# Optimization experiments

Hardware: AMD Instinct MI355X
Metric: run time of the kernel (lower is better)

The kernel has to match this reference:

```python
import jax, jax.numpy as jnp
import numpy as np
from jax import lax

A = 20            # len(ANCHOR_RATIOS)=4 * len(ANCHOR_SCALES)=5 in neural-motifs config
TGT = 6           # anchor_target_dim
DIM = 512
IN_DIM = 1024
B, H, W = 16, 37, 37


def setup_inputs() -> dict:
    key = jax.random.key(0)
    k1, k2, k3, k4, k5 = jax.random.split(key, 5)
    fmap = jax.random.normal(k1, (B, IN_DIM, H, W), dtype=jnp.float32)
    # conv weights in OIHW, fan-in scaled init
    W1 = jax.random.normal(k2, (DIM, IN_DIM, 3, 3), dtype=jnp.float32) / np.sqrt(IN_DIM * 9)
    b1 = jnp.zeros((DIM,), dtype=jnp.float32)
    W2 = jax.random.normal(k3, (TGT * A, DIM, 1, 1), dtype=jnp.float32) / np.sqrt(DIM)
    b2 = jnp.zeros((TGT * A,), dtype=jnp.float32)
    return {"fmap": fmap, "W1": W1, "b1": b1, "W2": W2, "b2": b2}


def reference(fmap, W1, b1, W2, b2):
    dn = ("NCHW", "OIHW", "NCHW")
    # 3x3 conv, padding=1
    x = lax.conv_general_dilated(fmap, W1, window_strides=(1, 1), padding="SAME",
                                 dimension_numbers=dn) + b1[None, :, None, None]
    # ReLU6
    x = jnp.clip(x, 0.0, 6.0)
    # 1x1 conv -> [B, 6*A, H, W]
    x = lax.conv_general_dilated(x, W2, window_strides=(1, 1), padding="VALID",
                                 dimension_numbers=dn) + b2[None, :, None, None]
    # _reshape_channels: [B, C, H, W] -> [B, H, W, C], then split C -> (A, 6)
    b, c, h, w = x.shape
    x = jnp.transpose(x, (0, 2, 3, 1))
    return x.reshape(b, h, w, A, TGT)
```

## Files before the change

kernel.cpp:

```cpp
#include <hip/hip_runtime.h>
#include <stdint.h>

#define HW   1369
#define QW   39
#define QP   1616
#define QT   1536
#define CIN  1024
#define CMID 512
#define KTOT 9216
#define NTIL 144
#define ASL  12288
#define BB   24576
#define BSL  8192

typedef float  f32x4  __attribute__((ext_vector_type(4)));
typedef __bf16 bf16x8 __attribute__((ext_vector_type(8)));

__device__ __forceinline__ uint16_t f2bf(float f) {
  uint32_t u = __float_as_uint(f);
  u += 0x7fffu + ((u >> 16) & 1u);
  return (uint16_t)(u >> 16);
}

__device__ __forceinline__ void gll16(const void* g, void* l) {
  const __attribute__((address_space(1))) uint32_t* ga =
      (const __attribute__((address_space(1))) uint32_t*)(uintptr_t)g;
  __attribute__((address_space(3))) uint32_t* la =
      (__attribute__((address_space(3))) uint32_t*)(uint32_t)(uintptr_t)l;
  __builtin_amdgcn_global_load_lds(ga, la, 16, 0, 0);
}

__global__ void k_zero_border(uint16_t* __restrict__ Xp) {
  const int bx = blockIdx.x;
  const int batch = bx / 210, idx = bx - batch * 210;
  int q;
  if (idx < 40)       q = idx;
  else if (idx < 136) q = 1520 + (idx - 40);
  else {
    const int k = idx - 136;
    const int pair = k >> 1;
    q = (k & 1) ? ((pair + 1) * 39 + 38)
                : ((pair + 2) * 39);
  }
  uint64_t* p = (uint64_t*)(Xp + ((size_t)batch * QP + q) * CIN);
  p[threadIdx.x] = 0ull;
}

__global__ void k_pad_transpose(const float* __restrict__ fmap, uint16_t* __restrict__ Xp) {
  __shared__ float t[32][33];
  const int b = blockIdx.z;
  const int c0 = blockIdx.y * 32;
  const int p0 = blockIdx.x * 32;
  const int tx = threadIdx.x, ty = threadIdx.y;
  const float* src = fmap + ((size_t)b * CIN + c0) * HW + p0;
#pragma unroll
  for (int i = 0; i < 4; ++i) {
    int cc = ty + i * 8;
    t[cc][tx] = (p0 + tx < HW) ? src[(size_t)cc * HW + tx] : 0.f;
  }
  __syncthreads();
#pragma unroll
  for (int i = 0; i < 4; ++i) {
    int pl = ty + i * 8;
    int p = p0 + pl;
    if (p < HW) {
      int h = p / 37, w = p - h * 37;
      int q = (h + 1) * QW + (w + 1);
      Xp[((size_t)b * QP + q) * CIN + c0 + tx] = f2bf(t[tx][pl]);
    }
  }
}

__global__ void k_pack_w1(const float* __restrict__ W1, uint16_t* __restrict__ Apk) {
  int idx = blockIdx.x * 256 + threadIdx.x;
  if (idx >= 512 * KTOT) return;
  int o = idx / KTOT, k = idx - o * KTOT;
  int r = k >> 10, c = k & 1023;
  Apk[idx] = f2bf(W1[((size_t)o * CIN + c) * 9 + r]);
}

__global__ void k_pack_w2(const float* __restrict__ W2, uint16_t* __restrict__ W2p) {
  int idx = blockIdx.x * 256 + threadIdx.x;
  int j = idx >> 9, o = idx & 511;
  W2p[idx] = (j < 120) ? f2bf(W2[j * 512 + o]) : (uint16_t)0;
}

__global__ __launch_bounds__(256, 2) void k_conv1(
    const uint16_t* __restrict__ Xp, const uint16_t* __restrict__ Apk,
    const float* __restrict__ b1, uint16_t* __restrict__ x1) {
  __shared__ __align__(16) uint16_t lds[2 * ASL + 2 * BSL];

  const int tid  = threadIdx.x;
  const int wid  = tid >> 6, lane = tid & 63;
  const int lrow = lane & 15, lq = lane >> 4;
  const int wm   = wid >> 1,  wn = wid & 1;

  const int bid = blockIdx.x;
  const int g   = (bid & 7) * 64 + (bid >> 3);
  const int mt  = g >> 2, nt = g & 3;
  const int batch = mt >> 3, qb = (mt & 7) * 192;
  const int o0 = nt * 128;
  const uint16_t* Xb = Xp + (size_t)batch * QP * CIN;

  const int xorb    = (lrow & 7) << 4;
  const int col_el0 = ((lq * 16) ^ xorb) >> 1;
  const int col_el1 = col_el0 ^ 32;

  const int scol = ((tid & 7) ^ ((tid >> 3) & 7)) * 8;
  const int srow = tid >> 3;

  f32x4 acc[6][4] = {};

#define STAGE(u) do {                                                                 \
    if ((u) < NTIL) {                                                                 \
      const int cb_  = (u) / 9;                                                       \
      const int tap_ = (u) - cb_ * 9;                                                 \
      const int off_ = (tap_ / 3) * QW + tap_ % 3;                                    \
      const int c0_  = cb_ << 6;                                                      \
      uint16_t* sa = lds + ((u) & 1) * ASL;                                           \
      uint16_t* sb = lds + BB + ((u) & 1) * BSL;                                      \
      _Pragma("unroll")                                                               \
      for (int j = 0; j < 6; ++j)                                                     \
        gll16(Xb + (size_t)(qb + off_ + j * 32 + srow) * CIN + c0_ + scol,            \
              sa + (j * 256 + wid * 64) * 8);                                         \
      _Pragma("unroll")                                                               \
      for (int j = 0; j < 4; ++j)                                                     \
        gll16(Apk + (size_t)(o0 + j * 32 + srow) * KTOT + (tap_ << 10) + c0_ + scol,  \
              sb + (j * 256 + wid * 64) * 8);                                         \
    }                                                                                 \
  } while (0)

  STAGE(0);

  for (int t = 0; t < NTIL; ++t) {
    const uint16_t* As = lds + (t & 1) * ASL;
    const uint16_t* Bs = lds + BB + (t & 1) * BSL;
    asm volatile("s_waitcnt vmcnt(0)" ::: "memory");
    asm volatile("s_barrier" ::: "memory");
    __builtin_amdgcn_sched_barrier(0);
    STAGE(t + 1);

    bf16x8 av0[6], av1[6], bv0[4], bv1[4];
#pragma unroll
    for (int n = 0; n < 4; ++n) {
      const uint16_t* br = Bs + (wn * 64 + n * 16 + lrow) * 64;
      bv0[n] = *(const bf16x8*)(br + col_el0);
      bv1[n] = *(const bf16x8*)(br + col_el1);
    }
#pragma unroll
    for (int m = 0; m < 6; ++m) {
      const uint16_t* ar = As + (wm * 96 + m * 16 + lrow) * 64;
      av0[m] = *(const bf16x8*)(ar + col_el0);
      av1[m] = *(const bf16x8*)(ar + col_el1);
    }
    __builtin_amdgcn_s_setprio(1);
#pragma unroll
    for (int m = 0; m < 6; ++m)
#pragma unroll
      for (int n = 0; n < 4; ++n)
        acc[m][n] = __builtin_amdgcn_mfma_f32_16x16x32_bf16(av0[m], bv0[n], acc[m][n], 0, 0, 0);
#pragma unroll
    for (int m = 0; m < 6; ++m)
#pragma unroll
      for (int n = 0; n < 4; ++n)
        acc[m][n] = __builtin_amdgcn_mfma_f32_16x16x32_bf16(av1[m], bv1[n], acc[m][n], 0, 0, 0);
    __builtin_amdgcn_s_setprio(0);
  }

  const int qr = lq * 4;
#pragma unroll
  for (int n = 0; n < 4; ++n) {
    const int o = o0 + wn * 64 + n * 16 + lrow;
    const float bias = b1[o];
#pragma unroll
    for (int m = 0; m < 6; ++m) {
#pragma unroll
      for (int v = 0; v < 4; ++v) {
        const int q = qb + wm * 96 + m * 16 + qr + v;
        float x = acc[m][n][v] + bias;
        x = fminf(fmaxf(x, 0.f), 6.f);
        x1[((size_t)batch * QT + q) * CMID + o] = f2bf(x);
      }
    }
  }
#undef STAGE
}

__global__ __launch_bounds__(256, 2) void k_conv2(
    const uint16_t* __restrict__ x1, const uint16_t* __restrict__ W2p,
    const float* __restrict__ b2, float* __restrict__ out) {
  __shared__ __align__(16) uint16_t lA[64 * 64];
  __shared__ __align__(16) uint16_t lB[128 * 64];
  const int tid = threadIdx.x;
  const int wid = tid >> 6, lane = tid & 63;
  const int b = blockIdx.z, q0 = blockIdx.x * 64;
  const uint16_t* Ab = x1 + (size_t)b * QT * CMID;
  const int wm = wid >> 1, wn = wid & 1;
  const int lrow = lane & 15, lk = (lane >> 4) * 8;
  f32x4 acc[2][4] = {};

  for (int kt = 0; kt < 8; ++kt) {
    const int c0 = kt << 6;
#pragma unroll
    for (int i = 0; i < 2; ++i) {
      int wb = i * 256 + wid * 64;
      int chunk = wb + lane;
      int row = chunk >> 3, ch = chunk & 7;
      gll16(Ab + (size_t)(q0 + row) * CMID + c0 + ch * 8, lA + wb * 8);
    }
#pragma unroll
    for (int i = 0; i < 4; ++i) {
      int wb = i * 256 + wid * 64;
      int chunk = wb + lane;
      int row = chunk >> 3, ch = chunk & 7;
      gll16(W2p + (size_t)row * CMID + c0 + ch * 8, lB + wb * 8);
    }
    __syncthreads();
#pragma unroll
    for (int kk = 0; kk < 2; ++kk) {
      bf16x8 av[2], bv[4];
#pragma unroll
      for (int mi = 0; mi < 2; ++mi)
        av[mi] = *(const bf16x8*)(lA + (wm * 32 + mi * 16 + lrow) * 64 + kk * 32 + lk);
#pragma unroll
      for (int ni = 0; ni < 4; ++ni)
        bv[ni] = *(const bf16x8*)(lB + (wn * 64 + ni * 16 + lrow) * 64 + kk * 32 + lk);
#pragma unroll
      for (int mi = 0; mi < 2; ++mi)
#pragma unroll
        for (int ni = 0; ni < 4; ++ni)
          acc[mi][ni] = __builtin_amdgcn_mfma_f32_16x16x32_bf16(av[mi], bv[ni], acc[mi][ni], 0, 0, 0);
    }
    __syncthreads();
  }

  const int qr = (lane >> 4) * 4;
#pragma unroll
  for (int ni = 0; ni < 4; ++ni) {
    int j = wn * 64 + ni * 16 + lrow;
    if (j < 120) {
      float bias = b2[j];
#pragma unroll
      for (int mi = 0; mi < 2; ++mi) {
#pragma unroll
        for (int v = 0; v < 4; ++v) {
          int q = q0 + wm * 32 + mi * 16 + qr + v;
          int h = q / QW, w = q - h * QW;
          if (h < 37 && w < 37) {
            out[((size_t)b * HW + h * 37 + w) * 120 + j] = acc[mi][ni][v] + bias;
          }
        }
      }
    }
  }
}

extern "C" void kernel_launch(void* const* d_in, const int* in_sizes, int n_in,
                              void* d_out, int out_size, void* d_ws, size_t ws_size,
                              hipStream_t stream) {
  const float* fmap = (const float*)d_in[0];
  const float* W1   = (const float*)d_in[1];
  const float* b1   = (const float*)d_in[2];
  const float* W2   = (const float*)d_in[3];
  const float* b2   = (const float*)d_in[4];
  float* out = (float*)d_out;

  uint8_t* ws = (uint8_t*)d_ws;
  const size_t XP_BYTES  = (size_t)16 * QP * CIN * 2;
  const size_t W1P_BYTES = (size_t)512 * KTOT * 2;
  const size_t W2P_BYTES = (size_t)128 * 512 * 2;
  uint16_t* Xp  = (uint16_t*)ws;
  uint16_t* Apk = (uint16_t*)(ws + XP_BYTES);
  uint16_t* W2p = (uint16_t*)(ws + XP_BYTES + W1P_BYTES);
  uint16_t* x1  = (uint16_t*)(ws + XP_BYTES + W1P_BYTES + W2P_BYTES);

  k_zero_border<<<dim3(16 * 210), dim3(256), 0, stream>>>(Xp);
  k_pad_transpose<<<dim3(43, 32, 16), dim3(32, 8), 0, stream>>>(fmap, Xp);
  k_pack_w1<<<dim3((512 * KTOT + 255) / 256), dim3(256), 0, stream>>>(W1, Apk);
  k_pack_w2<<<dim3(256), dim3(256), 0, stream>>>(W2, W2p);
  k_conv1<<<dim3(512), dim3(256), 0, stream>>>(Xp, Apk, b1, x1);
  k_conv2<<<dim3(24, 1, 16), dim3(256), 0, stream>>>(x1, W2p, b2, out);
}
```

Baseline: 242.9 us.

## Reuse a per-channel-block input panel across all nine conv taps

```diff
diff --git a/kernel.cpp b/kernel.cpp
--- a/kernel.cpp
+++ b/kernel.cpp
@@ -3,14 +3,13 @@
 
 #define HW   1369
 #define QW   39
-#define QP   1616
+#define QP2  1648
 #define QT   1536
 #define CIN  1024
 #define CMID 512
 #define KTOT 9216
 #define NTIL 144
-#define ASL  12288
-#define BB   24576
+#define PANEL 18432
 #define BSL  8192
 
 typedef float  f32x4  __attribute__((ext_vector_type(4)));
@@ -39,10 +38,9 @@
   else {
     const int k = idx - 136;
     const int pair = k >> 1;
-    q = (k & 1) ? ((pair + 1) * 39 + 38)
-                : ((pair + 2) * 39);
-  }
-  uint64_t* p = (uint64_t*)(Xp + ((size_t)batch * QP + q) * CIN);
+    q = (k & 1) ? ((pair + 1) * 39 + 38) : ((pair + 2) * 39);
+  }
+  uint64_t* p = (uint64_t*)(Xp + ((size_t)batch * QP2 + q) * CIN);
   p[threadIdx.x] = 0ull;
 }
 
@@ -66,7 +64,7 @@
     if (p < HW) {
       int h = p / 37, w = p - h * 37;
       int q = (h + 1) * QW + (w + 1);
-      Xp[((size_t)b * QP + q) * CIN + c0 + tx] = f2bf(t[tx][pl]);
+      Xp[((size_t)b * QP2 + q) * CIN + c0 + tx] = f2bf(t[tx][pl]);
     }
   }
 }
@@ -88,7 +86,7 @@
 __global__ __launch_bounds__(256, 2) void k_conv1(
     const uint16_t* __restrict__ Xp, const uint16_t* __restrict__ Apk,
     const float* __restrict__ b1, uint16_t* __restrict__ x1) {
-  __shared__ __align__(16) uint16_t lds[2 * ASL + 2 * BSL];
+  __shared__ __align__(16) uint16_t lds[PANEL + 2 * BSL];
 
   const int tid  = threadIdx.x;
   const int wid  = tid >> 6, lane = tid & 63;
@@ -100,7 +98,7 @@
   const int mt  = g >> 2, nt = g & 3;
   const int batch = mt >> 3, qb = (mt & 7) * 192;
   const int o0 = nt * 128;
-  const uint16_t* Xb = Xp + (size_t)batch * QP * CIN;
+  const uint16_t* Xb = Xp + (size_t)batch * QP2 * CIN;
 
   const int xorb    = (lrow & 7) << 4;
   const int col_el0 = ((lq * 16) ^ xorb) >> 1;
@@ -109,62 +107,83 @@
   const int scol = ((tid & 7) ^ ((tid >> 3) & 7)) * 8;
   const int srow = tid >> 3;
 
+  const int sR8 = lane >> 3;
+  const int sc8 = ((lane & 7) ^ sR8) * 8;
+
   f32x4 acc[6][4] = {};
 
-#define STAGE(u) do {                                                                 \
-    if ((u) < NTIL) {                                                                 \
-      const int cb_  = (u) / 9;                                                       \
-      const int tap_ = (u) - cb_ * 9;                                                 \
-      const int off_ = (tap_ / 3) * QW + tap_ % 3;                                    \
-      const int c0_  = cb_ << 6;                                                      \
-      uint16_t* sa = lds + ((u) & 1) * ASL;                                           \
-      uint16_t* sb = lds + BB + ((u) & 1) * BSL;                                      \
-      _Pragma("unroll")                                                               \
-      for (int j = 0; j < 6; ++j)                                                     \
-        gll16(Xb + (size_t)(qb + off_ + j * 32 + srow) * CIN + c0_ + scol,            \
-              sa + (j * 256 + wid * 64) * 8);                                         \
-      _Pragma("unroll")                                                               \
-      for (int j = 0; j < 4; ++j)                                                     \
-        gll16(Apk + (size_t)(o0 + j * 32 + srow) * KTOT + (tap_ << 10) + c0_ + scol,  \
-              sb + (j * 256 + wid * 64) * 8);                                         \
+#define STPAN(cb1, call) do {                                                         \
+    if ((cb1) < 16) {                                                                 \
+      const int c0_ = (cb1) << 6;                                                     \
+      const int Rb  = (call) * 32 + wid * 8;                                          \
+      gll16(Xb + (size_t)(qb + Rb + sR8) * CIN + c0_ + sc8, lds + Rb * 64);           \
     }                                                                                 \
   } while (0)
 
-  STAGE(0);
-
-  for (int t = 0; t < NTIL; ++t) {
-    const uint16_t* As = lds + (t & 1) * ASL;
-    const uint16_t* Bs = lds + BB + (t & 1) * BSL;
-    asm volatile("s_waitcnt vmcnt(0)" ::: "memory");
-    asm volatile("s_barrier" ::: "memory");
-    __builtin_amdgcn_sched_barrier(0);
-    STAGE(t + 1);
-
-    bf16x8 av0[6], av1[6], bv0[4], bv1[4];
-#pragma unroll
-    for (int n = 0; n < 4; ++n) {
-      const uint16_t* br = Bs + (wn * 64 + n * 16 + lrow) * 64;
-      bv0[n] = *(const bf16x8*)(br + col_el0);
-      bv1[n] = *(const bf16x8*)(br + col_el1);
-    }
-#pragma unroll
-    for (int m = 0; m < 6; ++m) {
-      const uint16_t* ar = As + (wm * 96 + m * 16 + lrow) * 64;
-      av0[m] = *(const bf16x8*)(ar + col_el0);
-      av1[m] = *(const bf16x8*)(ar + col_el1);
-    }
-    __builtin_amdgcn_s_setprio(1);
-#pragma unroll
-    for (int m = 0; m < 6; ++m)
-#pragma unroll
-      for (int n = 0; n < 4; ++n)
-        acc[m][n] = __builtin_amdgcn_mfma_f32_16x16x32_bf16(av0[m], bv0[n], acc[m][n], 0, 0, 0);
-#pragma unroll
-    for (int m = 0; m < 6; ++m)
-#pragma unroll
-      for (int n = 0; n < 4; ++n)
-        acc[m][n] = __builtin_amdgcn_mfma_f32_16x16x32_bf16(av1[m], bv1[n], acc[m][n], 0, 0, 0);
-    __builtin_amdgcn_s_setprio(0);
+#define STAGEB(cbv, tapv, slot) do {                                                  \
+    const int c0_ = (cbv) << 6;                                                       \
+    uint16_t* sb = lds + PANEL + (slot) * BSL;                                        \
+    _Pragma("unroll")                                                                 \
+    for (int j = 0; j < 4; ++j)                                                       \
+      gll16(Apk + (size_t)(o0 + j * 32 + srow) * KTOT + ((tapv) << 10) + c0_ + scol,  \
+            sb + (j * 256 + wid * 64) * 8);                                           \
+  } while (0)
+
+#pragma unroll
+  for (int c = 0; c < 9; ++c) STPAN(0, c);
+  STAGEB(0, 0, 0);
+
+  for (int cb = 0; cb < 16; ++cb) {
+#pragma unroll
+    for (int tap = 0; tap < 9; ++tap) {
+      const int t = cb * 9 + tap;
+      asm volatile("s_waitcnt vmcnt(0)" ::: "memory");
+      asm volatile("s_barrier" ::: "memory");
+      __builtin_amdgcn_sched_barrier(0);
+      if (tap < 8)           STAGEB(cb, tap + 1, (t + 1) & 1);
+      else if (cb + 1 < 16)  STAGEB(cb + 1, 0, (t + 1) & 1);
+
+      const int off_ = (tap / 3) * QW + tap % 3;
+      const int r7   = (off_ + lrow) & 7;
+      const int ce0  = ((lq * 16) ^ (r7 << 4)) >> 1;
+      const int ce1  = ce0 ^ 32;
+      const uint16_t* Bs = lds + PANEL + (t & 1) * BSL;
+
+      bf16x8 av0[6], av1[6], bv0[4], bv1[4];
+#pragma unroll
+      for (int n = 0; n < 4; ++n) {
+        const uint16_t* br = Bs + (wn * 64 + n * 16 + lrow) * 64;
+        bv0[n] = *(const bf16x8*)(br + col_el0);
+        bv1[n] = *(const bf16x8*)(br + col_el1);
+      }
+#pragma unroll
+      for (int m = 0; m < 6; ++m) {
+        const uint16_t* ar = lds + (off_ + wm * 96 + m * 16 + lrow) * 64;
+        av0[m] = *(const bf16x8*)(ar + ce0);
+        av1[m] = *(const bf16x8*)(ar + ce1);
+      }
+      __builtin_amdgcn_s_setprio(1);
+#pragma unroll
+      for (int m = 0; m < 6; ++m)
+#pragma unroll
+        for (int n = 0; n < 4; ++n)
+          acc[m][n] = __builtin_amdgcn_mfma_f32_16x16x32_bf16(av0[m], bv0[n], acc[m][n], 0, 0, 0);
+#pragma unroll
+      for (int m = 0; m < 6; ++m)
+#pragma unroll
+        for (int n = 0; n < 4; ++n)
+          acc[m][n] = __builtin_amdgcn_mfma_f32_16x16x32_bf16(av1[m], bv1[n], acc[m][n], 0, 0, 0);
+      __builtin_amdgcn_s_setprio(0);
+
+      if (tap == 8) {
+        asm volatile("s_barrier" ::: "memory");
+        __builtin_amdgcn_sched_barrier(0);
+        if (cb + 1 < 16) {
+#pragma unroll
+          for (int c = 0; c < 9; ++c) STPAN(cb + 1, c);
+        }
+      }
+    }
   }
 
   const int qr = lq * 4;
@@ -183,7 +202,8 @@
       }
     }
   }
-#undef STAGE
+#undef STAGEB
+#undef STPAN
 }
 
 __global__ __launch_bounds__(256, 2) void k_conv2(
@@ -266,7 +286,7 @@
   float* out = (float*)d_out;
 
   uint8_t* ws = (uint8_t*)d_ws;
-  const size_t XP_BYTES  = (size_t)16 * QP * CIN * 2;
+  const size_t XP_BYTES  = (size_t)16 * QP2 * CIN * 2;
   const size_t W1P_BYTES = (size_t)512 * KTOT * 2;
   const size_t W2P_BYTES = (size_t)128 * 512 * 2;
   uint16_t* Xp  = (uint16_t*)ws;
```

Result: faster. 230.7 us, median of 2 (-5.0%).
